# Kernel optimization log

Measured on AMD Instinct MI355X. Metric: run time of the kernel, lower is better.

Reference implementation:

```python
import jax, jax.numpy as jnp
import numpy as np

B, C, H, W = 8, 256, 128, 128
HEADS, DIM_HEAD = 4, 32
HID = HEADS * DIM_HEAD  # 128


def setup_inputs() -> dict:
    key = jax.random.key(0)
    k1, k2, k3, k4 = jax.random.split(key, 4)
    x = jax.random.normal(k1, (B, C, H, W), dtype=jnp.float32)
    # 1x1 conv weights stored as [out_ch, in_ch]
    w_qkv = jax.random.normal(k2, (3 * HID, C), dtype=jnp.float32) * (1.0 / np.sqrt(C))
    w_out = jax.random.normal(k3, (C, HID), dtype=jnp.float32) * (1.0 / np.sqrt(HID))
    b_out = jax.random.normal(k4, (C,), dtype=jnp.float32) * 0.01
    return {"x": x, "w_qkv": w_qkv, "w_out": w_out, "b_out": b_out}


def reference(x, w_qkv, w_out, b_out):
    b, c, h, w = x.shape
    n = h * w
    # 1x1 conv == channel matmul
    qkv = jnp.einsum('oc,bchw->bohw', w_qkv, x)  # [b, 3*HID, h, w]
    q, k, v = jnp.split(qkv, 3, axis=1)
    # rearrange 'b (heads d) h w -> b heads d (h w)'
    def to_heads(t):
        return t.reshape(b, HEADS, DIM_HEAD, n)
    q, k, v = to_heads(q), to_heads(k), to_heads(v)
    k = jax.nn.softmax(k, axis=-1)  # over spatial n
    # q_scale is False: q used as-is
    context = jnp.einsum('bhdn,bhen->bhde', k, v)   # [b, heads, d, e] small
    out = jnp.einsum('bhde,bhdn->bhen', context, q)  # [b, heads, e, n]
    out = out.reshape(b, HID, h, w)
    out = jnp.einsum('oc,bchw->bohw', w_out, out) + b_out[None, :, None, None]
    return out
```

## Files before the change

kernel.cpp:

```cpp
#include <hip/hip_runtime.h>
#include <stdint.h>

#define BB 8
#define CIN 256
#define NSP 16384
#define HID 128

typedef __bf16 bfrag __attribute__((ext_vector_type(8)));
typedef float  f32x4 __attribute__((ext_vector_type(4)));
typedef unsigned short us8 __attribute__((ext_vector_type(8)));

__device__ __forceinline__ unsigned short f2bf(float f) {
  union { float f; unsigned int u; } v; v.f = f;
  unsigned int u = v.u;
  return (unsigned short)((u + 0x7FFFu + ((u >> 16) & 1u)) >> 16);
}

__device__ __forceinline__ void gload_lds16(const unsigned short* g, unsigned short* l) {
  __builtin_amdgcn_global_load_lds((const __attribute__((address_space(1))) void*)g,
                                   (__attribute__((address_space(3))) void*)l, 16, 0, 0);
}

#define FENCE() asm volatile("" ::: "memory")

__global__ __launch_bounds__(256) void la_xT(const float* __restrict__ x,
                                             unsigned short* __restrict__ xT,
                                             const float* __restrict__ w_qkv,
                                             unsigned short* __restrict__ wkvb,
                                             float* __restrict__ zbase) {
  __shared__ float Xs[64][65];
  const int blk = blockIdx.x;
  const int t = threadIdx.x;
  if (blk < 8192) {
    const int b = blk >> 10;
    const int tile = blk & 1023;
    const int c0 = (tile & 3) * 64;
    const int n0 = (tile >> 2) * 64;
    const float* xb = x + (size_t)b * CIN * NSP;
    {
      const int c = t >> 2, nf = (t & 3) * 16;
      const float* xr = xb + (size_t)(c0 + c) * NSP + n0 + nf;
#pragma unroll
      for (int i = 0; i < 4; ++i) {
        const float4 v = *(const float4*)(xr + i * 4);
        Xs[c][nf + i * 4 + 0] = v.x;
        Xs[c][nf + i * 4 + 1] = v.y;
        Xs[c][nf + i * 4 + 2] = v.z;
        Xs[c][nf + i * 4 + 3] = v.w;
      }
    }
    __syncthreads();
    {
      const int n = t >> 2, c16 = (t & 3) * 16;
      us8 v0, v1;
#pragma unroll
      for (int j = 0; j < 8; ++j) {
        v0[j] = f2bf(Xs[c16 + j][n]);
        v1[j] = f2bf(Xs[c16 + 8 + j][n]);
      }
      unsigned short* orow = xT + ((size_t)b * NSP + n0 + n) * CIN + c0 + c16;
      *(us8*)orow = v0;
      *(us8*)(orow + 8) = v1;
    }
  } else if (blk < 8256) {
    const int off = ((blk - 8192) * 256 + t) * 4;
    const float4 wv4 = *(const float4*)(w_qkv + (size_t)128 * CIN + off);
    ushort4 p;
    p.x = f2bf(wv4.x); p.y = f2bf(wv4.y); p.z = f2bf(wv4.z); p.w = f2bf(wv4.w);
    *(ushort4*)(wkvb + off) = p;
  } else {
    for (int i = t; i < 8448; i += 256) {
      float4 z = {0.f, 0.f, 0.f, 0.f};
      *(float4*)(zbase + i * 4) = z;
    }
  }
}

__global__ __launch_bounds__(512, 4) void la_fused(const unsigned short* __restrict__ xT,
                                                   const unsigned short* __restrict__ wkvb,
                                                   float* __restrict__ ctxu,
                                                   float* __restrict__ sums) {
  __shared__ __align__(16) union {
    unsigned short Sx[4][4096];
    struct { unsigned short Lk[64][136]; unsigned short Lv[64][136];
             float Pc[4][1024]; } e;
  } sh;
  const int chunk = blockIdx.x;
  const int n0 = chunk * 128;
  const int b = blockIdx.y;
  const int t = threadIdx.x;
  const int lane = t & 63, wv = t >> 6;
  const int l15 = lane & 15, q = lane >> 4;
  const int qs = (q ^ ((l15 >> 1) & 3)) * 8;
  const unsigned short* xTb = xT + ((size_t)b * NSP + n0) * CIN;
  const int sn = t >> 2, sc8 = t & 3;
  const int sc8s = sc8 ^ ((sn >> 1) & 3);
  const unsigned short* sg = xTb + (size_t)sn * CIN + sc8s * 8;
  unsigned short* sl = &sh.Sx[0][0] + t * 8;
  f32x4 acc[2][8];
#pragma unroll
  for (int i = 0; i < 2; ++i)
#pragma unroll
    for (int j = 0; j < 8; ++j) acc[i][j] = 0.0f;

  gload_lds16(sg + 0 * 32, sl + 0 * 4096);
  gload_lds16(sg + 1 * 32, sl + 1 * 4096);
  asm volatile("s_waitcnt vmcnt(1)" ::: "memory");
  __builtin_amdgcn_s_barrier();
  FENCE();

#pragma unroll
  for (int kc = 0; kc < 6; ++kc) {
    bfrag a0 = *(const bfrag*)(wkvb + (size_t)(wv * 16 + l15) * CIN + kc * 32 + q * 8);
    bfrag a1 = *(const bfrag*)(wkvb + (size_t)(128 + wv * 16 + l15) * CIN + kc * 32 + q * 8);
    gload_lds16(sg + (kc + 2) * 32, sl + ((kc + 2) & 3) * 4096);
    const unsigned short* bufp = &sh.Sx[kc & 3][0];
#pragma unroll
    for (int ni = 0; ni < 8; ++ni) {
      bfrag bbv = *(const bfrag*)(bufp + (ni * 16 + l15) * 32 + qs);
      acc[0][ni] = __builtin_amdgcn_mfma_f32_16x16x32_bf16(a0, bbv, acc[0][ni], 0, 0, 0);
      acc[1][ni] = __builtin_amdgcn_mfma_f32_16x16x32_bf16(a1, bbv, acc[1][ni], 0, 0, 0);
    }
    asm volatile("s_waitcnt vmcnt(1)" ::: "memory");
    __builtin_amdgcn_s_barrier();
    FENCE();
  }
  {
    bfrag a0 = *(const bfrag*)(wkvb + (size_t)(wv * 16 + l15) * CIN + 6 * 32 + q * 8);
    bfrag a1 = *(const bfrag*)(wkvb + (size_t)(128 + wv * 16 + l15) * CIN + 6 * 32 + q * 8);
    const unsigned short* bufp = &sh.Sx[2][0];
#pragma unroll
    for (int ni = 0; ni < 8; ++ni) {
      bfrag bbv = *(const bfrag*)(bufp + (ni * 16 + l15) * 32 + qs);
      acc[0][ni] = __builtin_amdgcn_mfma_f32_16x16x32_bf16(a0, bbv, acc[0][ni], 0, 0, 0);
      acc[1][ni] = __builtin_amdgcn_mfma_f32_16x16x32_bf16(a1, bbv, acc[1][ni], 0, 0, 0);
    }
    asm volatile("s_waitcnt vmcnt(0)" ::: "memory");
    __builtin_amdgcn_s_barrier();
    FENCE();
  }
  {
    bfrag a0 = *(const bfrag*)(wkvb + (size_t)(wv * 16 + l15) * CIN + 7 * 32 + q * 8);
    bfrag a1 = *(const bfrag*)(wkvb + (size_t)(128 + wv * 16 + l15) * CIN + 7 * 32 + q * 8);
    const unsigned short* bufp = &sh.Sx[3][0];
#pragma unroll
    for (int ni = 0; ni < 8; ++ni) {
      bfrag bbv = *(const bfrag*)(bufp + (ni * 16 + l15) * 32 + qs);
      acc[0][ni] = __builtin_amdgcn_mfma_f32_16x16x32_bf16(a0, bbv, acc[0][ni], 0, 0, 0);
      acc[1][ni] = __builtin_amdgcn_mfma_f32_16x16x32_bf16(a1, bbv, acc[1][ni], 0, 0, 0);
    }
    __builtin_amdgcn_s_barrier();
    FENCE();
  }

#pragma unroll
  for (int ni = 0; ni < 8; ++ni)
#pragma unroll
    for (int rg = 0; rg < 4; ++rg) acc[0][ni][rg] = __expf(acc[0][ni][rg]);

  {
    float sp[4] = {0.f, 0.f, 0.f, 0.f};
#pragma unroll
    for (int ni = 0; ni < 8; ++ni)
#pragma unroll
      for (int rg = 0; rg < 4; ++rg) sp[rg] += acc[0][ni][rg];
#pragma unroll
    for (int rg = 0; rg < 4; ++rg) {
      float s = sp[rg];
      s += __shfl_down(s, 8, 16);
      s += __shfl_down(s, 4, 16);
      s += __shfl_down(s, 2, 16);
      s += __shfl_down(s, 1, 16);
      if (l15 == 0) atomicAdd(&sums[b * 128 + wv * 16 + q * 4 + rg], s);
    }
  }
#pragma unroll
  for (int ph = 0; ph < 2; ++ph) {
    if ((wv >> 2) == ph) {
      const int r = (wv & 3) * 16 + q * 4;
#pragma unroll
      for (int ni = 0; ni < 8; ++ni)
#pragma unroll
        for (int rg = 0; rg < 4; ++rg) {
          sh.e.Lk[r + rg][ni * 16 + l15] = f2bf(acc[0][ni][rg]);
          sh.e.Lv[r + rg][ni * 16 + l15] = f2bf(acc[1][ni][rg]);
        }
    }
    __syncthreads();
    const int hl = wv >> 2, nq = wv & 3;
    f32x4 c2[2][2];
    c2[0][0] = 0.f; c2[0][1] = 0.f; c2[1][0] = 0.f; c2[1][1] = 0.f;
    bfrag ka[2], vb[2];
#pragma unroll
    for (int d2 = 0; d2 < 2; ++d2)
      ka[d2] = *(const bfrag*)&sh.e.Lk[hl * 32 + d2 * 16 + l15][nq * 32 + q * 8];
#pragma unroll
    for (int e2 = 0; e2 < 2; ++e2)
      vb[e2] = *(const bfrag*)&sh.e.Lv[hl * 32 + e2 * 16 + l15][nq * 32 + q * 8];
#pragma unroll
    for (int d2 = 0; d2 < 2; ++d2)
#pragma unroll
      for (int e2 = 0; e2 < 2; ++e2)
        c2[d2][e2] = __builtin_amdgcn_mfma_f32_16x16x32_bf16(ka[d2], vb[e2], c2[d2][e2], 0, 0, 0);
    const int slot = hl * 2 + (nq & 1);
    if (nq < 2) {
#pragma unroll
      for (int d2 = 0; d2 < 2; ++d2)
#pragma unroll
        for (int e2 = 0; e2 < 2; ++e2)
#pragma unroll
          for (int rg = 0; rg < 4; ++rg)
            sh.e.Pc[slot][(d2 * 16 + q * 4 + rg) * 32 + e2 * 16 + l15] = c2[d2][e2][rg];
    }
    __syncthreads();
    if (nq >= 2) {
#pragma unroll
      for (int d2 = 0; d2 < 2; ++d2)
#pragma unroll
        for (int e2 = 0; e2 < 2; ++e2)
#pragma unroll
          for (int rg = 0; rg < 4; ++rg)
            sh.e.Pc[slot][(d2 * 16 + q * 4 + rg) * 32 + e2 * 16 + l15] += c2[d2][e2][rg];
    }
    __syncthreads();
    for (int idx = t; idx < 2048; idx += 512) {
      const int h2 = idx >> 10, pos = idx & 1023;
      atomicAdd(&ctxu[(size_t)b * 4096 + (ph * 2 + h2) * 1024 + pos],
                sh.e.Pc[h2 * 2][pos] + sh.e.Pc[h2 * 2 + 1][pos]);
    }
    __syncthreads();
  }
}

__global__ __launch_bounds__(256) void la_mid(const float* __restrict__ w_out,
                                              const float* __restrict__ ctxu,
                                              const float* __restrict__ sums,
                                              const float* __restrict__ w_qkv,
                                              unsigned short* __restrict__ wcomb) {
  __shared__ float wrow[128];
  const int o = blockIdx.x;
  const int b = blockIdx.y;
  const int t = threadIdx.x;
  if (t < 128) {
    const int h = t >> 5, d = t & 31;
    const float* wr = w_out + (size_t)o * HID + h * 32;
    const float* cr = ctxu + ((size_t)(b * 4 + h) * 32 + d) * 32;
    float s = 0.f;
#pragma unroll 8
    for (int e = 0; e < 32; ++e) s += wr[e] * cr[e];
    wrow[t] = s * (1.0f / sums[b * 128 + t]);
  }
  __syncthreads();
  float s = 0.f;
#pragma unroll 8
  for (int hd = 0; hd < 128; ++hd) s += wrow[hd] * w_qkv[(size_t)hd * CIN + t];
  wcomb[((size_t)b * 256 + o) * 256 + t] = f2bf(s);
}

__global__ __launch_bounds__(512, 4) void la_out(const unsigned short* __restrict__ wcomb,
                                                 const unsigned short* __restrict__ xT,
                                                 const float* __restrict__ b_out,
                                                 float* __restrict__ out) {
  __shared__ __align__(16) unsigned short Sx[4][4096];
  const int n0 = blockIdx.x * 128;
  const int b = blockIdx.y;
  const int t = threadIdx.x;
  const int lane = t & 63, wv = t >> 6;
  const int l15 = lane & 15, q = lane >> 4;
  const int qs = (q ^ ((l15 >> 1) & 3)) * 8;
  const int wm = (wv & 3) * 64;
  const int wn = (wv >> 2) * 64;
  const unsigned short* xTb = xT + ((size_t)b * NSP + n0) * CIN;
  const unsigned short* abase = wcomb + (size_t)b * 256 * 256;
  const int sn = t >> 2, sc8 = t & 3;
  const int sc8s = sc8 ^ ((sn >> 1) & 3);
  const unsigned short* sg = xTb + (size_t)sn * CIN + sc8s * 8;
  unsigned short* sl = &Sx[0][0] + t * 8;
  f32x4 acc[4][4];
#pragma unroll
  for (int i = 0; i < 4; ++i)
#pragma unroll
    for (int j = 0; j < 4; ++j) acc[i][j] = 0.0f;

  gload_lds16(sg + 0 * 32, sl + 0 * 4096);
  gload_lds16(sg + 1 * 32, sl + 1 * 4096);
  asm volatile("s_waitcnt vmcnt(1)" ::: "memory");
  __builtin_amdgcn_s_barrier();
  FENCE();

#pragma unroll
  for (int kc = 0; kc < 6; ++kc) {
    bfrag a[4];
#pragma unroll
    for (int mi = 0; mi < 4; ++mi)
      a[mi] = *(const bfrag*)(abase + (size_t)(wm + mi * 16 + l15) * 256 + kc * 32 + q * 8);
    gload_lds16(sg + (kc + 2) * 32, sl + ((kc + 2) & 3) * 4096);
    const unsigned short* bufp = &Sx[kc & 3][0];
#pragma unroll
    for (int ni = 0; ni < 4; ++ni) {
      bfrag bbv = *(const bfrag*)(bufp + (wn + ni * 16 + l15) * 32 + qs);
#pragma unroll
      for (int mi = 0; mi < 4; ++mi)
        acc[mi][ni] = __builtin_amdgcn_mfma_f32_16x16x32_bf16(a[mi], bbv, acc[mi][ni], 0, 0, 0);
    }
    asm volatile("s_waitcnt vmcnt(1)" ::: "memory");
    __builtin_amdgcn_s_barrier();
    FENCE();
  }
  {
    bfrag a[4];
#pragma unroll
    for (int mi = 0; mi < 4; ++mi)
      a[mi] = *(const bfrag*)(abase + (size_t)(wm + mi * 16 + l15) * 256 + 6 * 32 + q * 8);
    const unsigned short* bufp = &Sx[2][0];
#pragma unroll
    for (int ni = 0; ni < 4; ++ni) {
      bfrag bbv = *(const bfrag*)(bufp + (wn + ni * 16 + l15) * 32 + qs);
#pragma unroll
      for (int mi = 0; mi < 4; ++mi)
        acc[mi][ni] = __builtin_amdgcn_mfma_f32_16x16x32_bf16(a[mi], bbv, acc[mi][ni], 0, 0, 0);
    }
    asm volatile("s_waitcnt vmcnt(0)" ::: "memory");
    __builtin_amdgcn_s_barrier();
    FENCE();
  }
  {
    bfrag a[4];
#pragma unroll
    for (int mi = 0; mi < 4; ++mi)
      a[mi] = *(const bfrag*)(abase + (size_t)(wm + mi * 16 + l15) * 256 + 7 * 32 + q * 8);
    const unsigned short* bufp = &Sx[3][0];
#pragma unroll
    for (int ni = 0; ni < 4; ++ni) {
      bfrag bbv = *(const bfrag*)(bufp + (wn + ni * 16 + l15) * 32 + qs);
#pragma unroll
      for (int mi = 0; mi < 4; ++mi)
        acc[mi][ni] = __builtin_amdgcn_mfma_f32_16x16x32_bf16(a[mi], bbv, acc[mi][ni], 0, 0, 0);
    }
  }
  float* obase = out + (size_t)b * 256 * NSP;
#pragma unroll
  for (int mi = 0; mi < 4; ++mi) {
    const int ob = wm + mi * 16 + q * 4;
    const float4 bias = *(const float4*)(b_out + ob);
    float ba[4] = {bias.x, bias.y, bias.z, bias.w};
#pragma unroll
    for (int ni = 0; ni < 4; ++ni) {
      const int n = n0 + wn + ni * 16 + l15;
#pragma unroll
      for (int rg = 0; rg < 4; ++rg)
        obase[(size_t)(ob + rg) * NSP + n] = acc[mi][ni][rg] + ba[rg];
    }
  }
}


extern "C" void kernel_launch(void* const* d_in, const int* in_sizes, int n_in,
                              void* d_out, int out_size, void* d_ws, size_t ws_size,
                              hipStream_t stream) {
  (void)in_sizes; (void)n_in; (void)out_size; (void)ws_size;
  const float* x     = (const float*)d_in[0];
  const float* w_qkv = (const float*)d_in[1];
  const float* w_out = (const float*)d_in[2];
  const float* b_out = (const float*)d_in[3];
  float* out = (float*)d_out;
  char* ws = (char*)d_ws;
  unsigned short* xTws  = (unsigned short*)(ws);
  unsigned short* wkvb  = (unsigned short*)(ws + 67108864);
  float* ctxu           = (float*)(ws + 67239936);
  float* sums           = (float*)(ws + 67371008);
  unsigned short* wcomb = (unsigned short*)(ws + 67375104);

  la_xT<<<dim3(8257), dim3(256), 0, stream>>>(x, xTws, w_qkv, wkvb, ctxu);
  la_fused<<<dim3(NSP / 128, BB), dim3(512), 0, stream>>>(xTws, wkvb, ctxu, sums);
  la_mid<<<dim3(256, BB), dim3(256), 0, stream>>>(w_out, ctxu, sums, w_qkv, wcomb);
  la_out<<<dim3(NSP / 128, BB), dim3(512), 0, stream>>>(wcomb, xTws, b_out, out);
}
```

Baseline: 353.2 us.

## Fuse x transpose/bf16 conversion into the K/V projection pass

Removes the separate transpose kernel: pass1 now reads fp32 x directly, converts it to bf16 in a double-buffered LDS tile, writes the transposed bf16 copy for the output pass, and feeds the MFMA K/V projection from the same tile. The MMA orientation is flipped so spatial positions form the A operand and weights come straight from global memory. The context product is then computed from register fragments without an LDS round-trip, using a swizzled LDS reduction. This saves one full read of x in fp32 plus a kernel launch, but it loses the async global-to-LDS pipelining and adds weight reloads from global memory on every k-step.

```diff
diff --git a/kernel.cpp b/kernel.cpp
--- a/kernel.cpp
+++ b/kernel.cpp
@@ -16,6 +16,10 @@
   return (unsigned short)((u + 0x7FFFu + ((u >> 16) & 1u)) >> 16);
 }
 
+__device__ __forceinline__ bfrag us8_to_bfrag(us8 u) {
+  union { us8 u; bfrag b; } c; c.u = u; return c.b;
+}
+
 __device__ __forceinline__ void gload_lds16(const unsigned short* g, unsigned short* l) {
   __builtin_amdgcn_global_load_lds((const __attribute__((address_space(1))) void*)g,
                                    (__attribute__((address_space(3))) void*)l, 16, 0, 0);
@@ -23,47 +27,13 @@
 
 #define FENCE() asm volatile("" ::: "memory")
 
-__global__ __launch_bounds__(256) void la_xT(const float* __restrict__ x,
-                                             unsigned short* __restrict__ xT,
-                                             const float* __restrict__ w_qkv,
-                                             unsigned short* __restrict__ wkvb,
-                                             float* __restrict__ zbase) {
-  __shared__ float Xs[64][65];
+__global__ __launch_bounds__(256) void la_prep(const float* __restrict__ w_qkv,
+                                               unsigned short* __restrict__ wkvb,
+                                               float* __restrict__ zbase) {
   const int blk = blockIdx.x;
   const int t = threadIdx.x;
-  if (blk < 8192) {
-    const int b = blk >> 10;
-    const int tile = blk & 1023;
-    const int c0 = (tile & 3) * 64;
-    const int n0 = (tile >> 2) * 64;
-    const float* xb = x + (size_t)b * CIN * NSP;
-    {
-      const int c = t >> 2, nf = (t & 3) * 16;
-      const float* xr = xb + (size_t)(c0 + c) * NSP + n0 + nf;
-#pragma unroll
-      for (int i = 0; i < 4; ++i) {
-        const float4 v = *(const float4*)(xr + i * 4);
-        Xs[c][nf + i * 4 + 0] = v.x;
-        Xs[c][nf + i * 4 + 1] = v.y;
-        Xs[c][nf + i * 4 + 2] = v.z;
-        Xs[c][nf + i * 4 + 3] = v.w;
-      }
-    }
-    __syncthreads();
-    {
-      const int n = t >> 2, c16 = (t & 3) * 16;
-      us8 v0, v1;
-#pragma unroll
-      for (int j = 0; j < 8; ++j) {
-        v0[j] = f2bf(Xs[c16 + j][n]);
-        v1[j] = f2bf(Xs[c16 + 8 + j][n]);
-      }
-      unsigned short* orow = xT + ((size_t)b * NSP + n0 + n) * CIN + c0 + c16;
-      *(us8*)orow = v0;
-      *(us8*)(orow + 8) = v1;
-    }
-  } else if (blk < 8256) {
-    const int off = ((blk - 8192) * 256 + t) * 4;
+  if (blk < 64) {
+    const int off = (blk * 256 + t) * 4;
     const float4 wv4 = *(const float4*)(w_qkv + (size_t)128 * CIN + off);
     ushort4 p;
     p.x = f2bf(wv4.x); p.y = f2bf(wv4.y); p.z = f2bf(wv4.z); p.w = f2bf(wv4.w);
@@ -76,14 +46,14 @@
   }
 }
 
-__global__ __launch_bounds__(512, 4) void la_fused(const unsigned short* __restrict__ xT,
+__global__ __launch_bounds__(512, 4) void la_pass1(const float* __restrict__ x,
                                                    const unsigned short* __restrict__ wkvb,
+                                                   unsigned short* __restrict__ xT,
                                                    float* __restrict__ ctxu,
                                                    float* __restrict__ sums) {
   __shared__ __align__(16) union {
-    unsigned short Sx[4][4096];
-    struct { unsigned short Lk[64][136]; unsigned short Lv[64][136];
-             float Pc[4][1024]; } e;
+    struct { unsigned short Xb[2][128][40]; } g;
+    struct { float Pc[4][4096]; float Sw[8][128]; } e;
   } sh;
   const int chunk = blockIdx.x;
   const int n0 = chunk * 128;
@@ -91,144 +61,167 @@
   const int t = threadIdx.x;
   const int lane = t & 63, wv = t >> 6;
   const int l15 = lane & 15, q = lane >> 4;
-  const int qs = (q ^ ((l15 >> 1) & 3)) * 8;
-  const unsigned short* xTb = xT + ((size_t)b * NSP + n0) * CIN;
-  const int sn = t >> 2, sc8 = t & 3;
-  const int sc8s = sc8 ^ ((sn >> 1) & 3);
-  const unsigned short* sg = xTb + (size_t)sn * CIN + sc8s * 8;
-  unsigned short* sl = &sh.Sx[0][0] + t * 8;
-  f32x4 acc[2][8];
-#pragma unroll
-  for (int i = 0; i < 2; ++i)
-#pragma unroll
-    for (int j = 0; j < 8; ++j) acc[i][j] = 0.0f;
-
-  gload_lds16(sg + 0 * 32, sl + 0 * 4096);
-  gload_lds16(sg + 1 * 32, sl + 1 * 4096);
-  asm volatile("s_waitcnt vmcnt(1)" ::: "memory");
-  __builtin_amdgcn_s_barrier();
-  FENCE();
-
-#pragma unroll
-  for (int kc = 0; kc < 6; ++kc) {
-    bfrag a0 = *(const bfrag*)(wkvb + (size_t)(wv * 16 + l15) * CIN + kc * 32 + q * 8);
-    bfrag a1 = *(const bfrag*)(wkvb + (size_t)(128 + wv * 16 + l15) * CIN + kc * 32 + q * 8);
-    gload_lds16(sg + (kc + 2) * 32, sl + ((kc + 2) & 3) * 4096);
-    const unsigned short* bufp = &sh.Sx[kc & 3][0];
-#pragma unroll
-    for (int ni = 0; ni < 8; ++ni) {
-      bfrag bbv = *(const bfrag*)(bufp + (ni * 16 + l15) * 32 + qs);
-      acc[0][ni] = __builtin_amdgcn_mfma_f32_16x16x32_bf16(a0, bbv, acc[0][ni], 0, 0, 0);
-      acc[1][ni] = __builtin_amdgcn_mfma_f32_16x16x32_bf16(a1, bbv, acc[1][ni], 0, 0, 0);
-    }
-    asm volatile("s_waitcnt vmcnt(1)" ::: "memory");
-    __builtin_amdgcn_s_barrier();
-    FENCE();
-  }
-  {
-    bfrag a0 = *(const bfrag*)(wkvb + (size_t)(wv * 16 + l15) * CIN + 6 * 32 + q * 8);
-    bfrag a1 = *(const bfrag*)(wkvb + (size_t)(128 + wv * 16 + l15) * CIN + 6 * 32 + q * 8);
-    const unsigned short* bufp = &sh.Sx[2][0];
-#pragma unroll
-    for (int ni = 0; ni < 8; ++ni) {
-      bfrag bbv = *(const bfrag*)(bufp + (ni * 16 + l15) * 32 + qs);
-      acc[0][ni] = __builtin_amdgcn_mfma_f32_16x16x32_bf16(a0, bbv, acc[0][ni], 0, 0, 0);
-      acc[1][ni] = __builtin_amdgcn_mfma_f32_16x16x32_bf16(a1, bbv, acc[1][ni], 0, 0, 0);
-    }
-    asm volatile("s_waitcnt vmcnt(0)" ::: "memory");
-    __builtin_amdgcn_s_barrier();
-    FENCE();
-  }
-  {
-    bfrag a0 = *(const bfrag*)(wkvb + (size_t)(wv * 16 + l15) * CIN + 7 * 32 + q * 8);
-    bfrag a1 = *(const bfrag*)(wkvb + (size_t)(128 + wv * 16 + l15) * CIN + 7 * 32 + q * 8);
-    const unsigned short* bufp = &sh.Sx[3][0];
-#pragma unroll
-    for (int ni = 0; ni < 8; ++ni) {
-      bfrag bbv = *(const bfrag*)(bufp + (ni * 16 + l15) * 32 + qs);
-      acc[0][ni] = __builtin_amdgcn_mfma_f32_16x16x32_bf16(a0, bbv, acc[0][ni], 0, 0, 0);
-      acc[1][ni] = __builtin_amdgcn_mfma_f32_16x16x32_bf16(a1, bbv, acc[1][ni], 0, 0, 0);
-    }
-    __builtin_amdgcn_s_barrier();
-    FENCE();
-  }
-
-#pragma unroll
-  for (int ni = 0; ni < 8; ++ni)
-#pragma unroll
-    for (int rg = 0; rg < 4; ++rg) acc[0][ni][rg] = __expf(acc[0][ni][rg]);
-
-  {
-    float sp[4] = {0.f, 0.f, 0.f, 0.f};
-#pragma unroll
-    for (int ni = 0; ni < 8; ++ni)
-#pragma unroll
-      for (int rg = 0; rg < 4; ++rg) sp[rg] += acc[0][ni][rg];
-#pragma unroll
-    for (int rg = 0; rg < 4; ++rg) {
-      float s = sp[rg];
-      s += __shfl_down(s, 8, 16);
-      s += __shfl_down(s, 4, 16);
-      s += __shfl_down(s, 2, 16);
-      s += __shfl_down(s, 1, 16);
-      if (l15 == 0) atomicAdd(&sums[b * 128 + wv * 16 + q * 4 + rg], s);
-    }
-  }
-#pragma unroll
-  for (int ph = 0; ph < 2; ++ph) {
-    if ((wv >> 2) == ph) {
-      const int r = (wv & 3) * 16 + q * 4;
-#pragma unroll
-      for (int ni = 0; ni < 8; ++ni)
-#pragma unroll
-        for (int rg = 0; rg < 4; ++rg) {
-          sh.e.Lk[r + rg][ni * 16 + l15] = f2bf(acc[0][ni][rg]);
-          sh.e.Lv[r + rg][ni * 16 + l15] = f2bf(acc[1][ni][rg]);
+  const int cl = t & 31;
+  const int n16 = (t >> 5) * 8;
+  const float* xp = x + (size_t)b * CIN * NSP + n0;
+  unsigned short* xTb = xT + ((size_t)b * NSP + n0) * CIN;
+  f32x4 acc[16];
+#pragma unroll
+  for (int i = 0; i < 16; ++i) acc[i] = 0.0f;
+
+#define STOREX(B, A0, A1) do {                      \
+    sh.g.Xb[B][n16 + 0][cl] = f2bf((A0).x);         \
+    sh.g.Xb[B][n16 + 1][cl] = f2bf((A0).y);         \
+    sh.g.Xb[B][n16 + 2][cl] = f2bf((A0).z);         \
+    sh.g.Xb[B][n16 + 3][cl] = f2bf((A0).w);         \
+    sh.g.Xb[B][n16 + 4][cl] = f2bf((A1).x);         \
+    sh.g.Xb[B][n16 + 5][cl] = f2bf((A1).y);         \
+    sh.g.Xb[B][n16 + 6][cl] = f2bf((A1).z);         \
+    sh.g.Xb[B][n16 + 7][cl] = f2bf((A1).w);         \
+  } while (0)
+
+  float4 xa0, xa1;
+  {
+    const float* xr = xp + (size_t)cl * NSP + n16;
+    xa0 = *(const float4*)xr;
+    xa1 = *(const float4*)(xr + 4);
+  }
+  STOREX(0, xa0, xa1);
+  {
+    const float* xr = xp + (size_t)(32 + cl) * NSP + n16;
+    xa0 = *(const float4*)xr;
+    xa1 = *(const float4*)(xr + 4);
+  }
+  __syncthreads();
+
+#pragma unroll
+  for (int kc = 0; kc < 8; ++kc) {
+    const int buf = kc & 1;
+    if (kc < 7) {
+      STOREX(buf ^ 1, xa0, xa1);
+      if (kc < 6) {
+        const float* xr = xp + (size_t)((kc + 2) * 32 + cl) * NSP + n16;
+        xa0 = *(const float4*)xr;
+        xa1 = *(const float4*)(xr + 4);
+      }
+    }
+    {
+      const int rr = t >> 2, cc8 = (t & 3) * 8;
+      us8 wbv = *(const us8*)&sh.g.Xb[buf][rr][cc8];
+      *(us8*)(xTb + (size_t)rr * CIN + kc * 32 + cc8) = wbv;
+    }
+    bfrag af = *(const bfrag*)&sh.g.Xb[buf][wv * 16 + l15][q * 8];
+    const unsigned short* wbp = wkvb + (size_t)l15 * CIN + kc * 32 + q * 8;
+#pragma unroll
+    for (int cf = 0; cf < 16; ++cf) {
+      bfrag bv = *(const bfrag*)(wbp + (size_t)cf * 16 * CIN);
+      acc[cf] = __builtin_amdgcn_mfma_f32_16x16x32_bf16(af, bv, acc[cf], 0, 0, 0);
+    }
+    __syncthreads();
+  }
+#undef STOREX
+
+#pragma unroll
+  for (int cf = 0; cf < 8; ++cf)
+#pragma unroll
+    for (int rg = 0; rg < 4; ++rg) acc[cf][rg] = __expf(acc[cf][rg]);
+
+#pragma unroll
+  for (int cf = 0; cf < 8; ++cf) {
+    float s = acc[cf][0] + acc[cf][1] + acc[cf][2] + acc[cf][3];
+    s += __shfl_xor(s, 16);
+    s += __shfl_xor(s, 32);
+    if (q == 0) sh.e.Sw[wv][cf * 16 + l15] = s;
+  }
+
+  f32x4 ct[16];
+#pragma unroll
+  for (int i = 0; i < 16; ++i) ct[i] = 0.0f;
+#pragma unroll
+  for (int hh = 0; hh < 2; ++hh) {
+    bfrag kf[4], vf[4];
+#pragma unroll
+    for (int i = 0; i < 4; ++i) {
+      const int cf = hh * 4 + i;
+      us8 kt = {0, 0, 0, 0, 0, 0, 0, 0};
+      us8 vt = {0, 0, 0, 0, 0, 0, 0, 0};
+      kt[0] = f2bf(acc[cf][0]); kt[1] = f2bf(acc[cf][1]);
+      kt[2] = f2bf(acc[cf][2]); kt[3] = f2bf(acc[cf][3]);
+      vt[0] = f2bf(acc[8 + cf][0]); vt[1] = f2bf(acc[8 + cf][1]);
+      vt[2] = f2bf(acc[8 + cf][2]); vt[3] = f2bf(acc[8 + cf][3]);
+      kf[i] = us8_to_bfrag(kt);
+      vf[i] = us8_to_bfrag(vt);
+    }
+#pragma unroll
+    for (int hl = 0; hl < 2; ++hl)
+#pragma unroll
+      for (int dt = 0; dt < 2; ++dt)
+#pragma unroll
+        for (int et = 0; et < 2; ++et) {
+          const int tix = (hh * 2 + hl) * 4 + dt * 2 + et;
+          ct[tix] = __builtin_amdgcn_mfma_f32_16x16x32_bf16(kf[hl * 2 + dt], vf[hl * 2 + et],
+                                                            ct[tix], 0, 0, 0);
         }
+  }
+
+  {
+    const int slot = wv & 3;
+    float* pcs = sh.e.Pc[slot];
+    if (wv < 4) {
+#pragma unroll
+      for (int h = 0; h < 4; ++h)
+#pragma unroll
+        for (int dt = 0; dt < 2; ++dt)
+#pragma unroll
+          for (int et = 0; et < 2; ++et) {
+            const int e = et * 16 + l15;
+            const int sd = (dt * 16 + q * 4) ^ ((e & 7) << 2);
+            *(f32x4*)&pcs[h * 1024 + e * 32 + sd] = ct[h * 4 + dt * 2 + et];
+          }
     }
     __syncthreads();
-    const int hl = wv >> 2, nq = wv & 3;
-    f32x4 c2[2][2];
-    c2[0][0] = 0.f; c2[0][1] = 0.f; c2[1][0] = 0.f; c2[1][1] = 0.f;
-    bfrag ka[2], vb[2];
-#pragma unroll
-    for (int d2 = 0; d2 < 2; ++d2)
-      ka[d2] = *(const bfrag*)&sh.e.Lk[hl * 32 + d2 * 16 + l15][nq * 32 + q * 8];
-#pragma unroll
-    for (int e2 = 0; e2 < 2; ++e2)
-      vb[e2] = *(const bfrag*)&sh.e.Lv[hl * 32 + e2 * 16 + l15][nq * 32 + q * 8];
-#pragma unroll
-    for (int d2 = 0; d2 < 2; ++d2)
-#pragma unroll
-      for (int e2 = 0; e2 < 2; ++e2)
-        c2[d2][e2] = __builtin_amdgcn_mfma_f32_16x16x32_bf16(ka[d2], vb[e2], c2[d2][e2], 0, 0, 0);
-    const int slot = hl * 2 + (nq & 1);
-    if (nq < 2) {
-#pragma unroll
-      for (int d2 = 0; d2 < 2; ++d2)
-#pragma unroll
-        for (int e2 = 0; e2 < 2; ++e2)
-#pragma unroll
-          for (int rg = 0; rg < 4; ++rg)
-            sh.e.Pc[slot][(d2 * 16 + q * 4 + rg) * 32 + e2 * 16 + l15] = c2[d2][e2][rg];
+    if (wv >= 4) {
+#pragma unroll
+      for (int h = 0; h < 4; ++h)
+#pragma unroll
+        for (int dt = 0; dt < 2; ++dt)
+#pragma unroll
+          for (int et = 0; et < 2; ++et) {
+            const int e = et * 16 + l15;
+            const int sd = (dt * 16 + q * 4) ^ ((e & 7) << 2);
+            f32x4 o = *(const f32x4*)&pcs[h * 1024 + e * 32 + sd];
+            o += ct[h * 4 + dt * 2 + et];
+            *(f32x4*)&pcs[h * 1024 + e * 32 + sd] = o;
+          }
     }
     __syncthreads();
-    if (nq >= 2) {
-#pragma unroll
-      for (int d2 = 0; d2 < 2; ++d2)
-#pragma unroll
-        for (int e2 = 0; e2 < 2; ++e2)
-#pragma unroll
-          for (int rg = 0; rg < 4; ++rg)
-            sh.e.Pc[slot][(d2 * 16 + q * 4 + rg) * 32 + e2 * 16 + l15] += c2[d2][e2][rg];
-    }
-    __syncthreads();
-    for (int idx = t; idx < 2048; idx += 512) {
-      const int h2 = idx >> 10, pos = idx & 1023;
-      atomicAdd(&ctxu[(size_t)b * 4096 + (ph * 2 + h2) * 1024 + pos],
-                sh.e.Pc[h2 * 2][pos] + sh.e.Pc[h2 * 2 + 1][pos]);
-    }
-    __syncthreads();
+  }
+
+  if (t < 128) {
+    float s8 = 0.f;
+#pragma unroll
+    for (int w = 0; w < 8; ++w) s8 += sh.e.Sw[w][t];
+    atomicAdd(&sums[b * 128 + t], s8);
+  }
+  {
+    float* cub = ctxu + (size_t)b * 4096;
+    f32x4 v0 = {0.f, 0.f, 0.f, 0.f}, v1 = {0.f, 0.f, 0.f, 0.f};
+#pragma unroll
+    for (int s = 0; s < 4; ++s) {
+      v0 += *(const f32x4*)&sh.e.Pc[s][t * 4];
+      v1 += *(const f32x4*)&sh.e.Pc[s][2048 + t * 4];
+    }
+#pragma unroll
+    for (int j = 0; j < 4; ++j) {
+      int pos = t * 4 + j;
+      int h = pos >> 10, e = (pos >> 5) & 31, sd = pos & 31;
+      int d = sd ^ ((e & 7) << 2);
+      atomicAdd(&cub[(h * 32 + d) * 32 + e], v0[j]);
+      pos = 2048 + t * 4 + j;
+      h = pos >> 10; e = (pos >> 5) & 31; sd = pos & 31;
+      d = sd ^ ((e & 7) << 2);
+      atomicAdd(&cub[(h * 32 + d) * 32 + e], v1[j]);
+    }
   }
 }
 
@@ -371,8 +364,8 @@
   float* sums           = (float*)(ws + 67371008);
   unsigned short* wcomb = (unsigned short*)(ws + 67375104);
 
-  la_xT<<<dim3(8257), dim3(256), 0, stream>>>(x, xTws, w_qkv, wkvb, ctxu);
-  la_fused<<<dim3(NSP / 128, BB), dim3(512), 0, stream>>>(xTws, wkvb, ctxu, sums);
+  la_prep<<<dim3(65), dim3(256), 0, stream>>>(w_qkv, wkvb, ctxu);
+  la_pass1<<<dim3(NSP / 128, BB), dim3(512), 0, stream>>>(x, wkvb, xTws, ctxu, sums);
   la_mid<<<dim3(256, BB), dim3(256), 0, stream>>>(w_out, ctxu, sums, w_qkv, wcomb);
   la_out<<<dim3(NSP / 128, BB), dim3(512), 0, stream>>>(wcomb, xTws, b_out, out);
 }
```

Measured after the change: 399.9 us. 13.2% more time.
